# Performance work log

Hardware: AMD Instinct MI355X
Metric: run time of the kernel (lower is better)

The kernel has to match this reference:

```python
import jax, jax.numpy as jnp
import numpy as np

VOCAB = 8192
EMB = 80
UNITS = 2048
LAYERS = 6
BATCH = 64
SEQ = 64


def setup_inputs() -> dict:
    key = jax.random.key(0)
    ks = jax.random.split(key, 7)
    inputs = jax.random.randint(ks[0], (BATCH, SEQ), 0, VOCAB)
    emb = jax.random.normal(ks[1], (VOCAB, EMB), dtype=jnp.float32) * 0.05
    Wx = jax.random.normal(ks[2], (LAYERS, EMB, UNITS), dtype=jnp.float32) / np.sqrt(EMB)
    Wh = jax.random.normal(ks[3], (LAYERS, UNITS, UNITS), dtype=jnp.float32) / np.sqrt(UNITS)
    b = jnp.zeros((LAYERS, UNITS), dtype=jnp.float32)
    Wout = jax.random.normal(ks[4], (UNITS, 1), dtype=jnp.float32) / np.sqrt(UNITS)
    bout = jnp.zeros((1,), dtype=jnp.float32)
    return {"inputs": inputs, "emb": emb, "Wx": Wx, "Wh": Wh, "b": b, "Wout": Wout, "bout": bout}


def reference(inputs, emb, Wx, Wh, b, Wout, bout):
    # x: [B, T, EMB]
    x = emb[inputs]
    L = Wx.shape[0]
    B, U = inputs.shape[0], Wh.shape[-1]

    def step(states, xt):
        # states: [L, B, U]; xt: [B, EMB]
        # Faithful to original: every layer consumes xt and states[0],
        # and states[0] is updated before layers 1..L-1 read it.
        s0 = states[0]
        hs = []
        for i in range(L):
            h = jnp.tanh(xt @ Wx[i] + s0 @ Wh[i] + b[i])
            if i == 0:
                s0 = h
            hs.append(h)
        return jnp.stack(hs), None

    init = jnp.zeros((L, B, U), dtype=x.dtype)
    states, _ = jax.lax.scan(step, init, jnp.swapaxes(x, 0, 1))
    h_last = states[-1]  # last layer's output at final timestep, [B, U]
    return jax.nn.sigmoid(h_last @ Wout + bout)
```

## Files before the change

kernel.cpp:

```cpp
#include <hip/hip_runtime.h>
#include <math.h>

#define VOCABN 8192
#define EMBN   80
#define UNITSN 2048
#define BATCHN 64
#define SEQN   64

typedef _Float16 f16;
typedef _Float16 f16x8 __attribute__((ext_vector_type(8)));
typedef float    f32x4 __attribute__((ext_vector_type(4)));

#define BROW 4352

#define HBUF_BYTES   (2 * BATCHN * UNITSN * 2)
#define FLAGS_OFF    HBUF_BYTES
#define OUTPRE_OFF   (FLAGS_OFF + 4 * 64 * 4)
#define WS_ZERO_B    (OUTPRE_OFF + BATCHN * 4)

__device__ __forceinline__ f32x4 mfma16(f16x8 a, f16x8 b, f32x4 c) {
    return __builtin_amdgcn_mfma_f32_16x16x32_f16(a, b, c, 0, 0, 0);
}

__device__ __forceinline__ void bypass_load_b16(f16x8* dst, const void* p) {
    asm volatile("global_load_dwordx4 %0, %1, off sc0 sc1"
                 : "=v"(*dst) : "v"(p) : "memory");
}
__device__ __forceinline__ int bypass_load_b32(const void* p) {
    int r;
    asm volatile("global_load_dword %0, %1, off sc0 sc1\n\ts_waitcnt vmcnt(0)"
                 : "=v"(r) : "v"(p) : "memory");
    return r;
}
__device__ __forceinline__ void bypass_store_b32(void* p, unsigned int v) {
    asm volatile("global_store_dword %0, %1, off sc0 sc1"
                 :: "v"(p), "v"(v) : "memory");
}
__device__ __forceinline__ void wait_vm0(void) {
    asm volatile("s_waitcnt vmcnt(0)" ::: "memory");
    __builtin_amdgcn_sched_barrier(0);
}

__device__ __forceinline__ void load_wslice(const float* __restrict__ W,
                                            const float* __restrict__ Wxp,
                                            int c0, int tid, unsigned char* Blds)
{
    const int j0 = tid >> 3, l8 = tid & 7;
    for (int it = 0; it < 64; ++it) {
        const int j = j0 + it * 32;
        const float4 w = *(const float4*)(W + (size_t)j * UNITSN + c0 + l8 * 4);
        const float vals[4] = {w.x, w.y, w.z, w.w};
#pragma unroll
        for (int q = 0; q < 4; ++q) {
            const int uu = l8 * 4 + q;
            *(f16*)(Blds + uu * BROW + ((2 * j) ^ ((uu & 15) << 4))) = (f16)vals[q];
        }
    }
    for (int j2 = j0; j2 < 96; j2 += 32) {
        float vals[4] = {0.f, 0.f, 0.f, 0.f};
        if (j2 < EMBN) {
            const float4 w = *(const float4*)(Wxp + (size_t)j2 * UNITSN + c0 + l8 * 4);
            vals[0] = w.x; vals[1] = w.y; vals[2] = w.z; vals[3] = w.w;
        }
#pragma unroll
        for (int q = 0; q < 4; ++q) {
            const int uu = l8 * 4 + q;
            const int k = 2048 + j2;
            *(f16*)(Blds + uu * BROW + ((2 * k) ^ ((uu & 15) << 4))) = (f16)vals[q];
        }
    }
}

__global__ __launch_bounds__(256)
void rnn_recur(const int* __restrict__ inputs, const float* __restrict__ emb,
               const float* __restrict__ Wx, const float* __restrict__ Wh,
               const float* __restrict__ bias, f16* __restrict__ hbuf,
               int* __restrict__ flags)
{
    __shared__ unsigned char Blds[32 * BROW];
    __shared__ f16  xlds[2][16][96];
    __shared__ float red[4][2][64][4];
    __shared__ int  idxlds[16][SEQN];

    const int tid = threadIdx.x;
    const int wg  = blockIdx.x;
    const int g     = wg >> 6;
    const int wslot = wg & 63;
    const int c0  = wslot * 32;
    const int g16 = g * 16;

    for (int i = tid; i < 16 * SEQN; i += 256)
        idxlds[i >> 6][i & 63] = inputs[(g16 + (i >> 6)) * SEQN + (i & 63)];

    load_wslice(Wh, Wx, c0, tid, Blds);
    __syncthreads();

    {
        const int r  = tid >> 4;
        const int kb = (tid & 15) * 6;
        const float* erow = emb + (size_t)idxlds[r][0] * EMBN;
#pragma unroll
        for (int q = 0; q < 6; ++q) {
            const int k = kb + q;
            xlds[0][r][k] = (f16)((k < EMBN) ? erow[k] : 0.f);
        }
    }
    __syncthreads();

    const int lane = tid & 63;
    const int wv   = tid >> 6;
    const int l16  = lane & 15;
    const int lq   = lane >> 4;
    const int rr  = tid >> 4;
    const int cpa = (tid & 15) * 2;
    const float ba = bias[c0 + cpa];
    const float bb = bias[c0 + cpa + 1];
    const int tla = cpa >> 4;
    const int la  = ((rr >> 2) << 4) + (cpa & 15);
    const int rg  = rr & 3;

    int* gflags = flags + g * 64;

    for (int t = 0; t < SEQN; ++t) {
        const int p = t & 1;

        f32x4 acc0 = {0.f, 0.f, 0.f, 0.f};
        f32x4 acc1 = {0.f, 0.f, 0.f, 0.f};
        {
            const f16* hrow = hbuf + (size_t)p * BATCHN * UNITSN
                            + (size_t)(g16 + l16) * UNITSN + wv * 512 + lq * 8;
            const int swz = l16 << 4;
            const unsigned char* brow0 = Blds + l16 * BROW;
            const unsigned char* brow1 = Blds + (16 + l16) * BROW;
            f16x8 av[16];
#pragma unroll
            for (int kk = 0; kk < 16; ++kk)
                bypass_load_b16(&av[kk], hrow + kk * 32);
            f16x8 ax;
            if (wv < 3) ax = *(const f16x8*)(&xlds[p][l16][wv * 32 + lq * 8]);
            wait_vm0();
#pragma unroll
            for (int kk = 0; kk < 16; ++kk) {
                const int k0 = wv * 512 + kk * 32 + lq * 8;
                const int bo = (2 * k0) ^ swz;
                acc0 = mfma16(av[kk], *(const f16x8*)(brow0 + bo), acc0);
                acc1 = mfma16(av[kk], *(const f16x8*)(brow1 + bo), acc1);
            }
            if (wv < 3) {
                const int k0 = 2048 + wv * 32 + lq * 8;
                const int bo = (2 * k0) ^ swz;
                acc0 = mfma16(ax, *(const f16x8*)(brow0 + bo), acc0);
                acc1 = mfma16(ax, *(const f16x8*)(brow1 + bo), acc1);
            }
        }
        *(f32x4*)(&red[wv][0][lane][0]) = acc0;
        *(f32x4*)(&red[wv][1][lane][0]) = acc1;
        __syncthreads();

        {
            float va = ba, vb = bb;
#pragma unroll
            for (int w = 0; w < 4; ++w) {
                va += red[w][tla][la][rg];
                vb += red[w][tla][la + 1][rg];
            }
            const f16 ha = (f16)tanhf(va);
            const f16 hb = (f16)tanhf(vb);
            const unsigned int pk = (unsigned int)__builtin_bit_cast(unsigned short, ha)
                                  | ((unsigned int)__builtin_bit_cast(unsigned short, hb) << 16);
            unsigned int* dst = (unsigned int*)(hbuf + (size_t)(p ^ 1) * BATCHN * UNITSN
                                                + (size_t)(g16 + rr) * UNITSN + c0 + cpa);
            bypass_store_b32(dst, pk);
        }
        asm volatile("s_waitcnt vmcnt(0)" ::: "memory");
        __syncthreads();

        if (t == SEQN - 1) break;

        if (tid == 0)
            bypass_store_b32(&gflags[wslot], (unsigned int)(t + 1));

        {
            const int r  = tid >> 4;
            const int kb = (tid & 15) * 6;
            const float* erow = emb + (size_t)idxlds[r][t + 1] * EMBN;
            const int buf = (t + 1) & 1;
#pragma unroll
            for (int q = 0; q < 6; ++q) {
                const int k = kb + q;
                xlds[buf][r][k] = (f16)((k < EMBN) ? erow[k] : 0.f);
            }
        }

        if (wv == 0) {
            int tries = 0;
            for (;;) {
                const int v = bypass_load_b32(&gflags[lane]);
                if (__all(v > t)) break;
                __builtin_amdgcn_s_sleep(1);
                if (++tries > 150000) break;
            }
        }
        __syncthreads();
    }
}

__global__ __launch_bounds__(256)
void final_gemm(const int* __restrict__ inputs, const float* __restrict__ emb,
                const float* __restrict__ Wx, const float* __restrict__ Wh,
                const float* __restrict__ bias, const float* __restrict__ Wout,
                const f16* __restrict__ hbuf, float* __restrict__ out_pre)
{
    __shared__ unsigned char Blds[32 * BROW];
    __shared__ f16  xlds[64][96];
    __shared__ float red[4][64][4];
    __shared__ float rowacc[64][4];

    const int tid = threadIdx.x;
    const int c0  = blockIdx.x * 32;
    const float* Wh5 = Wh + (size_t)5 * UNITSN * UNITSN;
    const float* Wx5 = Wx + (size_t)5 * EMBN * UNITSN;
    const float* b5  = bias + 5 * UNITSN;

    load_wslice(Wh5, Wx5, c0, tid, Blds);
    {
        const int r  = tid >> 2;
        const int kb = (tid & 3) * 24;
        const float* erow = emb + (size_t)inputs[r * SEQN + SEQN - 1] * EMBN;
#pragma unroll
        for (int q = 0; q < 24; ++q) {
            const int k = kb + q;
            xlds[r][k] = (f16)((k < EMBN) ? erow[k] : 0.f);
        }
    }
    rowacc[tid >> 2][tid & 3] = 0.f;
    __syncthreads();

    const int lane = tid & 63;
    const int wv   = tid >> 6;
    const int l16  = lane & 15;
    const int lq   = lane >> 4;

    for (int ct = 0; ct < 2; ++ct) {
        f32x4 acc[4];
#pragma unroll
        for (int rt = 0; rt < 4; ++rt) acc[rt] = (f32x4){0.f, 0.f, 0.f, 0.f};
        const unsigned char* brow = Blds + (ct * 16 + l16) * BROW;
        const int swz = l16 << 4;
#pragma unroll
        for (int rt = 0; rt < 4; ++rt) {
            const f16* hrow = hbuf + (size_t)(rt * 16 + l16) * UNITSN + wv * 512 + lq * 8;
            f16x8 av[16];
#pragma unroll
            for (int kk = 0; kk < 16; ++kk)
                bypass_load_b16(&av[kk], hrow + kk * 32);
            f16x8 ax;
            if (wv < 3) ax = *(const f16x8*)(&xlds[rt * 16 + l16][wv * 32 + lq * 8]);
            wait_vm0();
#pragma unroll
            for (int kk = 0; kk < 16; ++kk) {
                const int k0 = wv * 512 + kk * 32 + lq * 8;
                acc[rt] = mfma16(av[kk], *(const f16x8*)(brow + ((2 * k0) ^ swz)), acc[rt]);
            }
            if (wv < 3) {
                const int k0 = 2048 + wv * 32 + lq * 8;
                acc[rt] = mfma16(ax, *(const f16x8*)(brow + ((2 * k0) ^ swz)), acc[rt]);
            }
        }
        if (wv == 0) {
#pragma unroll
            for (int rt = 0; rt < 4; ++rt) *(f32x4*)(&red[rt][lane][0]) = acc[rt];
        }
        __syncthreads();
#pragma unroll
        for (int w = 1; w < 4; ++w) {
            if (wv == w) {
#pragma unroll
                for (int rt = 0; rt < 4; ++rt) {
                    f32x4 cur = *(f32x4*)(&red[rt][lane][0]);
                    cur += acc[rt];
                    *(f32x4*)(&red[rt][lane][0]) = cur;
                }
            }
            __syncthreads();
        }
        {
            const int r = tid >> 2;
            float rsum = 0.f;
#pragma unroll
            for (int q = 0; q < 4; ++q) {
                const int cl = (tid & 3) * 4 + q;
                const int c  = ct * 16 + cl;
                const int lidx = (((r & 15) >> 2) << 4) + cl;
                float v = red[r >> 4][lidx][r & 3] + b5[c0 + c];
                v = tanhf(v);
                rsum += v * Wout[c0 + c];
            }
            rowacc[r][tid & 3] += rsum;
        }
        __syncthreads();
    }
    if (tid < 64) {
        const float s = rowacc[tid][0] + rowacc[tid][1] + rowacc[tid][2] + rowacc[tid][3];
        atomicAdd(&out_pre[tid], s);
    }
}

__global__ void final_out(const float* __restrict__ out_pre,
                          const float* __restrict__ bout, float* __restrict__ out)
{
    const int b = threadIdx.x;
    if (b < BATCHN) out[b] = 1.f / (1.f + expf(-(out_pre[b] + bout[0])));
}

extern "C" void kernel_launch(void* const* d_in, const int* in_sizes, int n_in,
                              void* d_out, int out_size, void* d_ws, size_t ws_size,
                              hipStream_t stream) {
    (void)in_sizes; (void)n_in; (void)out_size; (void)ws_size;
    const int*   inputs = (const int*)d_in[0];
    const float* emb    = (const float*)d_in[1];
    const float* Wx     = (const float*)d_in[2];
    const float* Wh     = (const float*)d_in[3];
    const float* bias   = (const float*)d_in[4];
    const float* Wout   = (const float*)d_in[5];
    const float* bout   = (const float*)d_in[6];
    float* out = (float*)d_out;

    f16*   hbuf    = (f16*)d_ws;
    int*   flags   = (int*)((char*)d_ws + FLAGS_OFF);
    float* out_pre = (float*)((char*)d_ws + OUTPRE_OFF);

    (void)hipMemsetAsync(d_ws, 0, WS_ZERO_B, stream);

    hipStreamCaptureStatus cs = hipStreamCaptureStatusNone;
    (void)hipStreamIsCapturing(stream, &cs);
    if (cs == hipStreamCaptureStatusActive) {
        rnn_recur<<<dim3(256), dim3(256), 0, stream>>>(inputs, emb, Wx, Wh, bias, hbuf, flags);
    } else {
        void* args[] = {(void*)&inputs, (void*)&emb, (void*)&Wx, (void*)&Wh,
                        (void*)&bias, (void*)&hbuf, (void*)&flags};
        hipError_t e = hipLaunchCooperativeKernel((const void*)rnn_recur, dim3(256), dim3(256),
                                                  args, 0, stream);
        if (e != hipSuccess) {
            rnn_recur<<<dim3(256), dim3(256), 0, stream>>>(inputs, emb, Wx, Wh, bias, hbuf, flags);
        }
    }
    final_gemm<<<dim3(64), dim3(256), 0, stream>>>(inputs, emb, Wx, Wh, bias, Wout, hbuf, out_pre);
    final_out<<<dim3(1), dim3(64), 0, stream>>>(out_pre, bout, out);
}
```

Before: 339.3 us.

## Halve recurrence grid by holding an extra weight slice in registers

Each workgroup of the persistent recurrence kernel now computes 64 output units instead of 32. The extra 32-column slice of Wh/Wx is preloaded from LDS into VGPRs and the other half stays in LDS, so the grid shrinks from 256 to 128 blocks and each flag barrier waits on 32 peers instead of 64. The goal is a cheaper per-step grid synchronisation and fewer participants, in exchange for twice the MFMA work per wave and heavy register pressure, with occupancy pinned to 1 via launch bounds. The final GEMM also switches from cache-bypassing loads to ordinary loads, and the inputs index is read directly instead of being staged in LDS.

```diff
diff --git a/kernel.cpp b/kernel.cpp
--- a/kernel.cpp
+++ b/kernel.cpp
@@ -10,12 +10,13 @@
 typedef _Float16 f16;
 typedef _Float16 f16x8 __attribute__((ext_vector_type(8)));
 typedef float    f32x4 __attribute__((ext_vector_type(4)));
+typedef unsigned int u32x2 __attribute__((ext_vector_type(2)));
 
 #define BROW 4352
 
 #define HBUF_BYTES   (2 * BATCHN * UNITSN * 2)
 #define FLAGS_OFF    HBUF_BYTES
-#define OUTPRE_OFF   (FLAGS_OFF + 4 * 64 * 4)
+#define OUTPRE_OFF   (FLAGS_OFF + 4 * 32 * 4)
 #define WS_ZERO_B    (OUTPRE_OFF + BATCHN * 4)
 
 __device__ __forceinline__ f32x4 mfma16(f16x8 a, f16x8 b, f32x4 c) {
@@ -36,9 +37,16 @@
     asm volatile("global_store_dword %0, %1, off sc0 sc1"
                  :: "v"(p), "v"(v) : "memory");
 }
+__device__ __forceinline__ void bypass_store_b64(void* p, u32x2 v) {
+    asm volatile("global_store_dwordx2 %0, %1, off sc0 sc1"
+                 :: "v"(p), "v"(v) : "memory");
+}
 __device__ __forceinline__ void wait_vm0(void) {
     asm volatile("s_waitcnt vmcnt(0)" ::: "memory");
     __builtin_amdgcn_sched_barrier(0);
+}
+__device__ __forceinline__ unsigned int us(f16 h) {
+    return (unsigned int)__builtin_bit_cast(unsigned short, h);
 }
 
 __device__ __forceinline__ void load_wslice(const float* __restrict__ W,
@@ -71,7 +79,7 @@
     }
 }
 
-__global__ __launch_bounds__(256)
+__global__ __launch_bounds__(256, 1)
 void rnn_recur(const int* __restrict__ inputs, const float* __restrict__ emb,
                const float* __restrict__ Wx, const float* __restrict__ Wh,
                const float* __restrict__ bias, f16* __restrict__ hbuf,
@@ -79,57 +87,76 @@
 {
     __shared__ unsigned char Blds[32 * BROW];
     __shared__ f16  xlds[2][16][96];
-    __shared__ float red[4][2][64][4];
-    __shared__ int  idxlds[16][SEQN];
+    __shared__ float red[4][4][64][4];
 
     const int tid = threadIdx.x;
     const int wg  = blockIdx.x;
-    const int g     = wg >> 6;
-    const int wslot = wg & 63;
-    const int c0  = wslot * 32;
+    const int g     = wg >> 5;
+    const int chunk = wg & 31;
+    const int c0  = chunk * 64;
     const int g16 = g * 16;
-
-    for (int i = tid; i < 16 * SEQN; i += 256)
-        idxlds[i >> 6][i & 63] = inputs[(g16 + (i >> 6)) * SEQN + (i & 63)];
-
-    load_wslice(Wh, Wx, c0, tid, Blds);
-    __syncthreads();
-
-    {
-        const int r  = tid >> 4;
-        const int kb = (tid & 15) * 6;
-        const float* erow = emb + (size_t)idxlds[r][0] * EMBN;
-#pragma unroll
-        for (int q = 0; q < 6; ++q) {
-            const int k = kb + q;
-            xlds[0][r][k] = (f16)((k < EMBN) ? erow[k] : 0.f);
-        }
-    }
-    __syncthreads();
 
     const int lane = tid & 63;
     const int wv   = tid >> 6;
     const int l16  = lane & 15;
     const int lq   = lane >> 4;
-    const int rr  = tid >> 4;
-    const int cpa = (tid & 15) * 2;
-    const float ba = bias[c0 + cpa];
-    const float bb = bias[c0 + cpa + 1];
-    const int tla = cpa >> 4;
-    const int la  = ((rr >> 2) << 4) + (cpa & 15);
-    const int rg  = rr & 3;
-
-    int* gflags = flags + g * 64;
+    const int swz  = l16 << 4;
+
+    f16x8 breg[16][2];
+    f16x8 bregx0 = {}, bregx1 = {};
+    load_wslice(Wh, Wx, c0 + 32, tid, Blds);
+    __syncthreads();
+    {
+        const unsigned char* brow0 = Blds + l16 * BROW;
+        const unsigned char* brow1 = Blds + (16 + l16) * BROW;
+#pragma unroll
+        for (int kk = 0; kk < 16; ++kk) {
+            const int k0 = wv * 512 + kk * 32 + lq * 8;
+            const int bo = (2 * k0) ^ swz;
+            breg[kk][0] = *(const f16x8*)(brow0 + bo);
+            breg[kk][1] = *(const f16x8*)(brow1 + bo);
+        }
+        if (wv < 3) {
+            const int k0 = 2048 + wv * 32 + lq * 8;
+            const int bo = (2 * k0) ^ swz;
+            bregx0 = *(const f16x8*)(brow0 + bo);
+            bregx1 = *(const f16x8*)(brow1 + bo);
+        }
+    }
+    __syncthreads();
+
+    load_wslice(Wh, Wx, c0, tid, Blds);
+
+    {
+        const int r  = tid >> 4;
+        const int kb = (tid & 15) * 6;
+        const float* erow = emb + (size_t)inputs[(g16 + r) * SEQN] * EMBN;
+#pragma unroll
+        for (int q = 0; q < 6; ++q) {
+            const int k = kb + q;
+            xlds[0][r][k] = (f16)((k < EMBN) ? erow[k] : 0.f);
+        }
+    }
+    __syncthreads();
+
+    const int rr = tid >> 4;
+    const int cb = (tid & 15) * 4;
+    float bias4[4];
+#pragma unroll
+    for (int q = 0; q < 4; ++q) bias4[q] = bias[c0 + cb + q];
+
+    int* gflags = flags + g * 32;
 
     for (int t = 0; t < SEQN; ++t) {
         const int p = t & 1;
 
         f32x4 acc0 = {0.f, 0.f, 0.f, 0.f};
         f32x4 acc1 = {0.f, 0.f, 0.f, 0.f};
+        f32x4 acc2 = {0.f, 0.f, 0.f, 0.f};
+        f32x4 acc3 = {0.f, 0.f, 0.f, 0.f};
         {
             const f16* hrow = hbuf + (size_t)p * BATCHN * UNITSN
                             + (size_t)(g16 + l16) * UNITSN + wv * 512 + lq * 8;
-            const int swz = l16 << 4;
             const unsigned char* brow0 = Blds + l16 * BROW;
             const unsigned char* brow1 = Blds + (16 + l16) * BROW;
             f16x8 av[16];
@@ -145,32 +172,44 @@
                 const int bo = (2 * k0) ^ swz;
                 acc0 = mfma16(av[kk], *(const f16x8*)(brow0 + bo), acc0);
                 acc1 = mfma16(av[kk], *(const f16x8*)(brow1 + bo), acc1);
+                acc2 = mfma16(av[kk], breg[kk][0], acc2);
+                acc3 = mfma16(av[kk], breg[kk][1], acc3);
             }
             if (wv < 3) {
                 const int k0 = 2048 + wv * 32 + lq * 8;
                 const int bo = (2 * k0) ^ swz;
                 acc0 = mfma16(ax, *(const f16x8*)(brow0 + bo), acc0);
                 acc1 = mfma16(ax, *(const f16x8*)(brow1 + bo), acc1);
+                acc2 = mfma16(ax, bregx0, acc2);
+                acc3 = mfma16(ax, bregx1, acc3);
             }
         }
         *(f32x4*)(&red[wv][0][lane][0]) = acc0;
         *(f32x4*)(&red[wv][1][lane][0]) = acc1;
+        *(f32x4*)(&red[wv][2][lane][0]) = acc2;
+        *(f32x4*)(&red[wv][3][lane][0]) = acc3;
         __syncthreads();
 
         {
-            float va = ba, vb = bb;
-#pragma unroll
-            for (int w = 0; w < 4; ++w) {
-                va += red[w][tla][la][rg];
-                vb += red[w][tla][la + 1][rg];
-            }
-            const f16 ha = (f16)tanhf(va);
-            const f16 hb = (f16)tanhf(vb);
-            const unsigned int pk = (unsigned int)__builtin_bit_cast(unsigned short, ha)
-                                  | ((unsigned int)__builtin_bit_cast(unsigned short, hb) << 16);
-            unsigned int* dst = (unsigned int*)(hbuf + (size_t)(p ^ 1) * BATCHN * UNITSN
-                                                + (size_t)(g16 + rr) * UNITSN + c0 + cpa);
-            bypass_store_b32(dst, pk);
+            float vv[4];
+#pragma unroll
+            for (int q = 0; q < 4; ++q) {
+                const int c  = cb + q;
+                const int tl = c >> 4;
+                const int la = ((rr >> 2) << 4) | (c & 15);
+                const int rg = rr & 3;
+                float s = bias4[q];
+#pragma unroll
+                for (int w = 0; w < 4; ++w)
+                    s += red[w][tl][la][rg];
+                vv[q] = tanhf(s);
+            }
+            u32x2 pk;
+            pk[0] = us((f16)vv[0]) | (us((f16)vv[1]) << 16);
+            pk[1] = us((f16)vv[2]) | (us((f16)vv[3]) << 16);
+            char* dst = (char*)(hbuf + (size_t)(p ^ 1) * BATCHN * UNITSN
+                                + (size_t)(g16 + rr) * UNITSN + c0 + cb);
+            bypass_store_b64(dst, pk);
         }
         asm volatile("s_waitcnt vmcnt(0)" ::: "memory");
         __syncthreads();
@@ -178,12 +217,12 @@
         if (t == SEQN - 1) break;
 
         if (tid == 0)
-            bypass_store_b32(&gflags[wslot], (unsigned int)(t + 1));
+            bypass_store_b32(&gflags[chunk], (unsigned int)(t + 1));
 
         {
             const int r  = tid >> 4;
             const int kb = (tid & 15) * 6;
-            const float* erow = emb + (size_t)idxlds[r][t + 1] * EMBN;
+            const float* erow = emb + (size_t)inputs[(g16 + r) * SEQN + t + 1] * EMBN;
             const int buf = (t + 1) & 1;
 #pragma unroll
             for (int q = 0; q < 6; ++q) {
@@ -195,7 +234,7 @@
         if (wv == 0) {
             int tries = 0;
             for (;;) {
-                const int v = bypass_load_b32(&gflags[lane]);
+                const int v = bypass_load_b32(&gflags[lane & 31]);
                 if (__all(v > t)) break;
                 __builtin_amdgcn_s_sleep(1);
                 if (++tries > 150000) break;
@@ -253,10 +292,9 @@
             f16x8 av[16];
 #pragma unroll
             for (int kk = 0; kk < 16; ++kk)
-                bypass_load_b16(&av[kk], hrow + kk * 32);
+                av[kk] = *(const f16x8*)(hrow + kk * 32);
             f16x8 ax;
             if (wv < 3) ax = *(const f16x8*)(&xlds[rt * 16 + l16][wv * 32 + lq * 8]);
-            wait_vm0();
 #pragma unroll
             for (int kk = 0; kk < 16; ++kk) {
                 const int k0 = wv * 512 + kk * 32 + lq * 8;
@@ -335,14 +373,14 @@
     hipStreamCaptureStatus cs = hipStreamCaptureStatusNone;
     (void)hipStreamIsCapturing(stream, &cs);
     if (cs == hipStreamCaptureStatusActive) {
-        rnn_recur<<<dim3(256), dim3(256), 0, stream>>>(inputs, emb, Wx, Wh, bias, hbuf, flags);
+        rnn_recur<<<dim3(128), dim3(256), 0, stream>>>(inputs, emb, Wx, Wh, bias, hbuf, flags);
     } else {
         void* args[] = {(void*)&inputs, (void*)&emb, (void*)&Wx, (void*)&Wh,
                         (void*)&bias, (void*)&hbuf, (void*)&flags};
-        hipError_t e = hipLaunchCooperativeKernel((const void*)rnn_recur, dim3(256), dim3(256),
+        hipError_t e = hipLaunchCooperativeKernel((const void*)rnn_recur, dim3(128), dim3(256),
                                                   args, 0, stream);
         if (e != hipSuccess) {
-            rnn_recur<<<dim3(256), dim3(256), 0, stream>>>(inputs, emb, Wx, Wh, bias, hbuf, flags);
+            rnn_recur<<<dim3(128), dim3(256), 0, stream>>>(inputs, emb, Wx, Wh, bias, hbuf, flags);
         }
     }
     final_gemm<<<dim3(64), dim3(256), 0, stream>>>(inputs, emb, Wx, Wh, bias, Wout, hbuf, out_pre);
```

Measured after the change: 409.8 us. 20.8% more time.
